# Kernel tuning notes

Measured on AMD Instinct MI355X. Metric: run time of the kernel, lower is better.

## Reference

```python
import math
import jax, jax.numpy as jnp
import numpy as np

B, M, L, H = 8, 2048, 2048, 1024


def setup_inputs() -> dict:
    key = jax.random.key(0)
    k1, k2, k3, k4 = jax.random.split(key, 4)
    return {
        "query": jax.random.normal(k1, (B, M, H), dtype=jnp.float32),
        "key": jax.random.normal(k2, (B, L, H), dtype=jnp.float32),
        "value": jax.random.normal(k3, (B, L, H), dtype=jnp.float32),
        "key_pe": jax.random.normal(k4, (1, H, L), dtype=jnp.float32),
        "hidden_size": H,
    }


def reference(query, key, value, key_pe, hidden_size):
    # content scores: [B, M, L]
    attn_cont = jnp.einsum("bmh,blh->bml", query, key)
    # relative-position scores: [B, M, H] @ [1, H, L] -> [B, M, L]
    attn_pos = jnp.matmul(query, key_pe)
    # NOTE: the original module computes softmax(attn)+dropout but then
    # (as written) multiplies VALUE by the raw content scores, not the
    # softmaxed attention. We reproduce that math faithfully; the softmax
    # is dead code w.r.t. the output (kept here for documentation, DCE'd by jit).
    attn = jax.nn.softmax((attn_cont + attn_pos) / math.sqrt(hidden_size), axis=-1)  # noqa: F841
    # dropout: identity in eval mode (and unused for the output anyway)
    out = jnp.matmul(attn_cont, value)  # [B, M, H]
    return out
```

## Files before the change

kernel.cpp:

```cpp
#include <hip/hip_runtime.h>
#include <hip/hip_bf16.h>


typedef __bf16 bf16x8 __attribute__((ext_vector_type(8)));
typedef float f32x4 __attribute__((ext_vector_type(4)));
typedef unsigned short u16_t;

#define GLD_LDS16(g, l)                                                        \
  __builtin_amdgcn_global_load_lds(                                            \
      (const __attribute__((address_space(1))) void*)(g),                      \
      (__attribute__((address_space(3))) void*)(l), 16, 0, 0)

static __device__ inline u16_t f2b(float x) {
  __hip_bfloat16 h = __float2bfloat16(x);
  u16_t u;
  __builtin_memcpy(&u, &h, 2);
  return u;
}
static __device__ inline unsigned pack2(float a, float b) {
  return (unsigned)f2b(a) | ((unsigned)f2b(b) << 16);
}
static __device__ inline float b2f(u16_t u) {
  unsigned v = (unsigned)u << 16;
  float f;
  __builtin_memcpy(&f, &v, 4);
  return f;
}

__global__ __launch_bounds__(256) void transpose_kv(
    const float* __restrict__ Kin, const float* __restrict__ Vin,
    u16_t* __restrict__ Kt, u16_t* __restrict__ Vt, int L, int Hd, int ldT) {
  __shared__ unsigned tile[64][260];
  const int bz = blockIdx.z;
  const float* in = (bz < 8) ? Kin : Vin;
  u16_t* out = (bz < 8) ? Kt : Vt;
  const int batch = bz & 7;
  in += (size_t)batch * (size_t)L * Hd;
  out += (size_t)batch * (size_t)Hd * ldT;
  const int h0 = blockIdx.x * 64;
  const int l0 = blockIdx.y * 512;

  const int tid = threadIdx.x;
  const int h4 = (tid & 15) * 4;
  const int lp0 = tid >> 4;

#pragma unroll
  for (int g = 0; g < 4; ++g) {
    float4 r0[4], r1[4];
#pragma unroll
    for (int it = 0; it < 4; ++it) {
      const int lp = lp0 + 16 * (4 * g + it);
      const int l = l0 + 2 * lp;
      r0[it] = *(const float4*)(in + (size_t)l * Hd + h0 + h4);
      r1[it] = *(const float4*)(in + (size_t)(l + 1) * Hd + h0 + h4);
    }
#pragma unroll
    for (int it = 0; it < 4; ++it) {
      const int lp = lp0 + 16 * (4 * g + it);
      tile[h4 + 0][lp] = pack2(r0[it].x, r1[it].x);
      tile[h4 + 1][lp] = pack2(r0[it].y, r1[it].y);
      tile[h4 + 2][lp] = pack2(r0[it].z, r1[it].z);
      tile[h4 + 3][lp] = pack2(r0[it].w, r1[it].w);
    }
  }
  __syncthreads();

  const int wv = tid >> 6;
  const int lane = tid & 63;
#pragma unroll
  for (int r = 0; r < 16; ++r) {
    const int h = wv * 16 + r;
    unsigned u[4];
#pragma unroll
    for (int j = 0; j < 4; ++j) u[j] = tile[h][4 * lane + j];
    *(uint4*)(out + (size_t)(h0 + h) * ldT + l0 + lane * 8) = *(const uint4*)u;
  }
}

static __device__ inline void store_c(float* p, float v) { *p = v; }
static __device__ inline void store_c(u16_t* p, float v) { *p = f2b(v); }

template <typename OutT>
static __device__ inline void gemm256_body(
    const u16_t* __restrict__ A, const u16_t* __restrict__ Bt,
    OutT* __restrict__ C, int N, int K, int ldA, int ldB,
    long sA, long sB, long sC, int tile_shift, long sCsplit) {
  __shared__ __align__(16) u16_t As[2][256 * 64];
  __shared__ __align__(16) u16_t Bs[2][256 * 64];

  const int batch = blockIdx.x & 7;
  const unsigned u = blockIdx.x >> 3;
  const int kh = (int)(u >> tile_shift);
  const unsigned t = u & ((1u << tile_shift) - 1u);
  const int m0 = (int)(t >> 2) * 256;
  const int n0 = (int)(t & 3) * 256;

  A  += (size_t)batch * (size_t)sA + (size_t)kh * (size_t)K;
  Bt += (size_t)batch * (size_t)sB + (size_t)kh * (size_t)K;
  C  += (size_t)batch * (size_t)sC + (size_t)kh * (size_t)sCsplit;

  const int tid = threadIdx.x;
  const int lane = tid & 63;
  const int w  = tid >> 6;
  const int wm = w & 1;
  const int wn = w >> 1;
  const int s  = lane & 15;
  const int q  = lane >> 4;
  const int s7 = s & 7;

  const u16_t* gA[4];
  const u16_t* gB[4];
  int lofs[4];
#pragma unroll
  for (int j = 0; j < 4; ++j) {
    const int i = tid + 512 * j;
    const int row = i >> 3;
    const int gchunk = (i & 7) ^ (row & 7);
    gA[j] = A  + (size_t)(m0 + row) * ldA + gchunk * 8;
    gB[j] = Bt + (size_t)(n0 + row) * ldB + gchunk * 8;
    lofs[j] = i * 8;
  }

  f32x4 acc[8][4];
#pragma unroll
  for (int r = 0; r < 8; ++r)
#pragma unroll
    for (int c = 0; c < 4; ++c) acc[r][c] = (f32x4){0.f, 0.f, 0.f, 0.f};

  auto STAGE = [&](u16_t* dA, u16_t* dB, int k0) {
#pragma unroll
    for (int j = 0; j < 4; ++j) GLD_LDS16(gA[j] + k0, dA + lofs[j]);
#pragma unroll
    for (int j = 0; j < 4; ++j) GLD_LDS16(gB[j] + k0, dB + lofs[j]);
  };

  auto COMPUTE = [&](const u16_t* As_, const u16_t* Bs_) {
#pragma unroll
    for (int kk = 0; kk < 2; ++kk) {
      const int slot = (kk * 4 + q) ^ s7;
      bf16x8 bfr[4];
#pragma unroll
      for (int c = 0; c < 4; ++c)
        bfr[c] = *(const bf16x8*)(Bs_ + (64 * wn + 16 * c + s) * 64 + slot * 8);
#pragma unroll
      for (int r = 0; r < 8; ++r) {
        const bf16x8 af =
            *(const bf16x8*)(As_ + (128 * wm + 16 * r + s) * 64 + slot * 8);
#pragma unroll
        for (int c = 0; c < 4; ++c)
          acc[r][c] = __builtin_amdgcn_mfma_f32_16x16x32_bf16(af, bfr[c],
                                                              acc[r][c], 0, 0, 0);
      }
    }
  };

  const int nt = K / 64;
  STAGE(As[0], Bs[0], 0);
  __syncthreads();
  for (int tt = 0; tt < nt; tt += 2) {
    if (tt + 1 < nt) STAGE(As[1], Bs[1], (tt + 1) * 64);
    COMPUTE(As[0], Bs[0]);
    __syncthreads();
    if (tt + 2 < nt) STAGE(As[0], Bs[0], (tt + 2) * 64);
    COMPUTE(As[1], Bs[1]);
    __syncthreads();
  }

#pragma unroll
  for (int r = 0; r < 8; ++r) {
#pragma unroll
    for (int c = 0; c < 4; ++c) {
      const int col = n0 + 64 * wn + 16 * c + s;
#pragma unroll
      for (int e = 0; e < 4; ++e) {
        const int row = m0 + 128 * wm + 16 * r + q * 4 + e;
        store_c(&C[(size_t)row * N + col], acc[r][c][e]);
      }
    }
  }
}

__global__ __launch_bounds__(512) void gemm1_kv(
    const u16_t* __restrict__ Vt, const u16_t* __restrict__ Kt,
    u16_t* __restrict__ W0, int N, int K, int ld, long sA, long sB, long sC,
    long sCsplit) {
  gemm256_body<u16_t>(Vt, Kt, W0, N, K, ld, ld, sA, sB, sC, 4, sCsplit);
}

__global__ __launch_bounds__(512) void gemm2_qw(
    const u16_t* __restrict__ Qb, const u16_t* __restrict__ Wb,
    float* __restrict__ C, int N, int K, long sA, long sB, long sC) {
  gemm256_body<float>(Qb, Wb, C, N, K, K, K, sA, sB, sC, 5, 0);
}

__global__ __launch_bounds__(256) void qcvt_wsum(
    const float* __restrict__ Q, const u16_t* __restrict__ W0,
    const u16_t* __restrict__ W1, u16_t* __restrict__ Qb,
    u16_t* __restrict__ Wb, size_t nQbatch, size_t nWbatch) {
  const int batch = blockIdx.y;
  if (blockIdx.z == 0) {
    const size_t base = (size_t)batch * nWbatch +
                        (size_t)blockIdx.x * 2048 + threadIdx.x * 8;
    const uint4 u0 = *(const uint4*)(W0 + base);
    const uint4 u1 = *(const uint4*)(W1 + base);
    const u16_t* p0 = (const u16_t*)&u0;
    const u16_t* p1 = (const u16_t*)&u1;
    u16_t o[8];
#pragma unroll
    for (int j = 0; j < 8; ++j) o[j] = f2b(b2f(p0[j]) + b2f(p1[j]));
    *(uint4*)(Wb + base) = *(const uint4*)o;
  } else {
    const size_t base = (size_t)batch * nQbatch +
                        (size_t)blockIdx.x * 4096 + threadIdx.x * 16;
    const float* src = Q + base;
    u16_t* dst = Qb + base;
#pragma unroll
    for (int half = 0; half < 2; ++half) {
      const float4 a = *(const float4*)(src + half * 8);
      const float4 b = *(const float4*)(src + half * 8 + 4);
      unsigned o[4] = {pack2(a.x, a.y), pack2(a.z, a.w),
                       pack2(b.x, b.y), pack2(b.z, b.w)};
      *(uint4*)(dst + half * 8) = *(const uint4*)o;
    }
  }
}

extern "C" void kernel_launch(void* const* d_in, const int* in_sizes, int n_in,
                              void* d_out, int out_size, void* d_ws, size_t ws_size,
                              hipStream_t stream) {
  const int B = 8, M = 2048, L = 2048, H = 1024;
  const int ldT = L + 16;

  const float* q = (const float*)d_in[0];
  const float* k = (const float*)d_in[1];
  const float* v = (const float*)d_in[2];

  const size_t nKtP = (size_t)B * H * ldT;
  const size_t nW   = (size_t)B * H * H;
  const size_t need = (2 * nKtP + 2 * nW) * sizeof(u16_t);
  if (ws_size < need) return;

  u16_t* Kt = (u16_t*)d_ws;
  u16_t* Vt = Kt + nKtP;
  u16_t* W0 = Vt + nKtP;
  u16_t* W1 = W0 + nW;
  u16_t* Qb = Kt;
  u16_t* Wb = Vt;

  transpose_kv<<<dim3(H / 64, L / 512, 16), dim3(256), 0, stream>>>(
      k, v, Kt, Vt, L, H, ldT);

  gemm1_kv<<<dim3(B * 16 * 2), dim3(512), 0, stream>>>(
      Vt, Kt, W0, H, L / 2, ldT, (long)H * ldT, (long)H * ldT, (long)H * H,
      (long)B * H * H);

  qcvt_wsum<<<dim3(512, B, 2), dim3(256), 0, stream>>>(
      q, W0, W1, Qb, Wb, (size_t)M * H, (size_t)H * H);

  gemm2_qw<<<dim3(B * 32), dim3(512), 0, stream>>>(
      Qb, Wb, (float*)d_out, H, H, (long)M * H, (long)H * H, (long)M * H);
}
```

Measured before the change: 308.9 us.

## Store transposed K/V in 32-wide L panels for contiguous transpose writes

The K/V transpose now writes bf16 output in panel layout: for each 32-row chunk of L, a contiguous [H][32] block. Each block handles one full 32-row panel across all H, so both global reads and writes are fully contiguous. The panel-aware GEMM1 addressing reads 64-wide K slices as two 32-wide panels. This removes strided row writes and padding in the transpose but makes GEMM1's global-to-LDS loads more fragmented across panels.

```diff
diff --git a/kernel.cpp b/kernel.cpp
--- a/kernel.cpp
+++ b/kernel.cpp
@@ -29,61 +29,61 @@
 
 __global__ __launch_bounds__(256) void transpose_kv(
     const float* __restrict__ Kin, const float* __restrict__ Vin,
-    u16_t* __restrict__ Kt, u16_t* __restrict__ Vt, int L, int Hd, int ldT) {
-  __shared__ unsigned tile[64][260];
+    u16_t* __restrict__ Kt, u16_t* __restrict__ Vt, int L, int Hd) {
+  __shared__ unsigned tile[1024 * 17];
   const int bz = blockIdx.z;
   const float* in = (bz < 8) ? Kin : Vin;
   u16_t* out = (bz < 8) ? Kt : Vt;
   const int batch = bz & 7;
-  in += (size_t)batch * (size_t)L * Hd;
-  out += (size_t)batch * (size_t)Hd * ldT;
-  const int h0 = blockIdx.x * 64;
-  const int l0 = blockIdx.y * 512;
+  const int p = blockIdx.x;
+  in  += (size_t)batch * L * Hd + (size_t)p * 32 * Hd;
+  out += (size_t)batch * L * Hd + (size_t)p * 32 * Hd;
 
   const int tid = threadIdx.x;
-  const int h4 = (tid & 15) * 4;
-  const int lp0 = tid >> 4;
+  const int swz = (tid + (tid >> 4)) & 15;
 
 #pragma unroll
   for (int g = 0; g < 4; ++g) {
-    float4 r0[4], r1[4];
-#pragma unroll
-    for (int it = 0; it < 4; ++it) {
-      const int lp = lp0 + 16 * (4 * g + it);
-      const int l = l0 + 2 * lp;
-      r0[it] = *(const float4*)(in + (size_t)l * Hd + h0 + h4);
-      r1[it] = *(const float4*)(in + (size_t)(l + 1) * Hd + h0 + h4);
-    }
-#pragma unroll
-    for (int it = 0; it < 4; ++it) {
-      const int lp = lp0 + 16 * (4 * g + it);
-      tile[h4 + 0][lp] = pack2(r0[it].x, r1[it].x);
-      tile[h4 + 1][lp] = pack2(r0[it].y, r1[it].y);
-      tile[h4 + 2][lp] = pack2(r0[it].z, r1[it].z);
-      tile[h4 + 3][lp] = pack2(r0[it].w, r1[it].w);
+    float4 a[4], b[4];
+#pragma unroll
+    for (int uu = 0; uu < 4; ++uu) {
+      const int u = g * 4 + uu;
+      a[uu] = *(const float4*)(in + (size_t)(2 * u) * Hd + tid * 4);
+      b[uu] = *(const float4*)(in + (size_t)(2 * u + 1) * Hd + tid * 4);
+    }
+#pragma unroll
+    for (int uu = 0; uu < 4; ++uu) {
+      const int u = g * 4 + uu;
+      const int col = u ^ swz;
+      tile[(4 * tid + 0) * 17 + col] = pack2(a[uu].x, b[uu].x);
+      tile[(4 * tid + 1) * 17 + col] = pack2(a[uu].y, b[uu].y);
+      tile[(4 * tid + 2) * 17 + col] = pack2(a[uu].z, b[uu].z);
+      tile[(4 * tid + 3) * 17 + col] = pack2(a[uu].w, b[uu].w);
     }
   }
   __syncthreads();
 
-  const int wv = tid >> 6;
-  const int lane = tid & 63;
-#pragma unroll
-  for (int r = 0; r < 16; ++r) {
-    const int h = wv * 16 + r;
-    unsigned u[4];
-#pragma unroll
-    for (int j = 0; j < 4; ++j) u[j] = tile[h][4 * lane + j];
-    *(uint4*)(out + (size_t)(h0 + h) * ldT + l0 + lane * 8) = *(const uint4*)u;
+  const int c = tid & 3;
+  const int hr = tid >> 2;
+#pragma unroll
+  for (int g = 0; g < 16; ++g) {
+    const int h = g * 64 + hr;
+    const int t = h >> 2;
+    const int s = (t + (t >> 4)) & 15;
+    unsigned dw[4];
+#pragma unroll
+    for (int j = 0; j < 4; ++j) dw[j] = tile[h * 17 + ((4 * c + j) ^ s)];
+    *(uint4*)(out + (size_t)h * 32 + c * 8) = *(const uint4*)dw;
   }
 }
 
 static __device__ inline void store_c(float* p, float v) { *p = v; }
 static __device__ inline void store_c(u16_t* p, float v) { *p = f2b(v); }
 
-template <typename OutT>
+template <typename OutT, bool PANEL>
 static __device__ inline void gemm256_body(
     const u16_t* __restrict__ A, const u16_t* __restrict__ Bt,
-    OutT* __restrict__ C, int N, int K, int ldA, int ldB,
+    OutT* __restrict__ C, int N, int K,
     long sA, long sB, long sC, int tile_shift, long sCsplit) {
   __shared__ __align__(16) u16_t As[2][256 * 64];
   __shared__ __align__(16) u16_t Bs[2][256 * 64];
@@ -95,8 +95,10 @@
   const int m0 = (int)(t >> 2) * 256;
   const int n0 = (int)(t & 3) * 256;
 
-  A  += (size_t)batch * (size_t)sA + (size_t)kh * (size_t)K;
-  Bt += (size_t)batch * (size_t)sB + (size_t)kh * (size_t)K;
+  A  += (size_t)batch * (size_t)sA +
+        (PANEL ? (size_t)kh * (size_t)K * 1024 : (size_t)kh * (size_t)K);
+  Bt += (size_t)batch * (size_t)sB +
+        (PANEL ? (size_t)kh * (size_t)K * 1024 : (size_t)kh * (size_t)K);
   C  += (size_t)batch * (size_t)sC + (size_t)kh * (size_t)sCsplit;
 
   const int tid = threadIdx.x;
@@ -116,8 +118,15 @@
     const int i = tid + 512 * j;
     const int row = i >> 3;
     const int gchunk = (i & 7) ^ (row & 7);
-    gA[j] = A  + (size_t)(m0 + row) * ldA + gchunk * 8;
-    gB[j] = Bt + (size_t)(n0 + row) * ldB + gchunk * 8;
+    if constexpr (PANEL) {
+      gA[j] = A  + (size_t)(gchunk >> 2) * 32768 + (size_t)(m0 + row) * 32 +
+              (gchunk & 3) * 8;
+      gB[j] = Bt + (size_t)(gchunk >> 2) * 32768 + (size_t)(n0 + row) * 32 +
+              (gchunk & 3) * 8;
+    } else {
+      gA[j] = A  + (size_t)(m0 + row) * K + gchunk * 8;
+      gB[j] = Bt + (size_t)(n0 + row) * K + gchunk * 8;
+    }
     lofs[j] = i * 8;
   }
 
@@ -128,10 +137,11 @@
     for (int c = 0; c < 4; ++c) acc[r][c] = (f32x4){0.f, 0.f, 0.f, 0.f};
 
   auto STAGE = [&](u16_t* dA, u16_t* dB, int k0) {
-#pragma unroll
-    for (int j = 0; j < 4; ++j) GLD_LDS16(gA[j] + k0, dA + lofs[j]);
-#pragma unroll
-    for (int j = 0; j < 4; ++j) GLD_LDS16(gB[j] + k0, dB + lofs[j]);
+    const size_t ko = PANEL ? (size_t)k0 * 1024 : (size_t)k0;
+#pragma unroll
+    for (int j = 0; j < 4; ++j) GLD_LDS16(gA[j] + ko, dA + lofs[j]);
+#pragma unroll
+    for (int j = 0; j < 4; ++j) GLD_LDS16(gB[j] + ko, dB + lofs[j]);
   };
 
   auto COMPUTE = [&](const u16_t* As_, const u16_t* Bs_) {
@@ -182,15 +192,15 @@
 
 __global__ __launch_bounds__(512) void gemm1_kv(
     const u16_t* __restrict__ Vt, const u16_t* __restrict__ Kt,
-    u16_t* __restrict__ W0, int N, int K, int ld, long sA, long sB, long sC,
+    u16_t* __restrict__ W0, int N, int K, long sA, long sB, long sC,
     long sCsplit) {
-  gemm256_body<u16_t>(Vt, Kt, W0, N, K, ld, ld, sA, sB, sC, 4, sCsplit);
+  gemm256_body<u16_t, true>(Vt, Kt, W0, N, K, sA, sB, sC, 4, sCsplit);
 }
 
 __global__ __launch_bounds__(512) void gemm2_qw(
     const u16_t* __restrict__ Qb, const u16_t* __restrict__ Wb,
     float* __restrict__ C, int N, int K, long sA, long sB, long sC) {
-  gemm256_body<float>(Qb, Wb, C, N, K, K, K, sA, sB, sC, 5, 0);
+  gemm256_body<float, false>(Qb, Wb, C, N, K, sA, sB, sC, 5, 0);
 }
 
 __global__ __launch_bounds__(256) void qcvt_wsum(
@@ -229,29 +239,27 @@
                               void* d_out, int out_size, void* d_ws, size_t ws_size,
                               hipStream_t stream) {
   const int B = 8, M = 2048, L = 2048, H = 1024;
-  const int ldT = L + 16;
 
   const float* q = (const float*)d_in[0];
   const float* k = (const float*)d_in[1];
   const float* v = (const float*)d_in[2];
 
-  const size_t nKtP = (size_t)B * H * ldT;
-  const size_t nW   = (size_t)B * H * H;
-  const size_t need = (2 * nKtP + 2 * nW) * sizeof(u16_t);
+  const size_t nKt = (size_t)B * H * L;
+  const size_t nW  = (size_t)B * H * H;
+  const size_t need = (2 * nKt + 2 * nW) * sizeof(u16_t);
   if (ws_size < need) return;
 
   u16_t* Kt = (u16_t*)d_ws;
-  u16_t* Vt = Kt + nKtP;
-  u16_t* W0 = Vt + nKtP;
+  u16_t* Vt = Kt + nKt;
+  u16_t* W0 = Vt + nKt;
   u16_t* W1 = W0 + nW;
   u16_t* Qb = Kt;
   u16_t* Wb = Vt;
 
-  transpose_kv<<<dim3(H / 64, L / 512, 16), dim3(256), 0, stream>>>(
-      k, v, Kt, Vt, L, H, ldT);
+  transpose_kv<<<dim3(L / 32, 1, 16), dim3(256), 0, stream>>>(k, v, Kt, Vt, L, H);
 
   gemm1_kv<<<dim3(B * 16 * 2), dim3(512), 0, stream>>>(
-      Vt, Kt, W0, H, L / 2, ldT, (long)H * ldT, (long)H * ldT, (long)H * H,
+      Vt, Kt, W0, H, L / 2, (long)H * L, (long)H * L, (long)H * H,
       (long)B * H * H);
 
   qcvt_wsum<<<dim3(512, B, 2), dim3(256), 0, stream>>>(
```

Result: faster. 300.9 us (-2.6%).
